# Optimization experiments

Measured on AMD Instinct MI355X. Metric: run time of the kernel, lower is better.

The kernel has to match this reference:

```python
import jax, jax.numpy as jnp
import numpy as np

N = 50000; E = 1600000; H = 128; R = 8; T = 2; P = 1000; M = 223


def setup_inputs() -> dict:
    key = jax.random.key(0)
    ks = jax.random.split(key, 16)
    s = 1.0 / np.sqrt(H).astype(np.float32)
    inp = {}
    inp['neigh_type_count'] = jax.random.uniform(ks[0], (N, 2), dtype=jnp.float32) * 5.0
    inp['norm'] = jax.random.uniform(ks[1], (E,), dtype=jnp.float32) + 0.1
    inp['special_cost'] = jax.random.uniform(ks[2], (N,), dtype=jnp.float32)
    inp['gt_map'] = jax.random.uniform(ks[3], (M, M), dtype=jnp.float32)
    inp['fc_w'] = jax.random.normal(ks[4], (2, H), dtype=jnp.float32) * (1.0 / np.sqrt(2.0))
    inp['fc_b'] = jnp.zeros((H,), jnp.float32)
    inp['w_nt'] = jax.random.normal(ks[5], (T, H, H), dtype=jnp.float32) * s
    inp['w_rel'] = jax.random.normal(ks[6], (R, H, H), dtype=jnp.float32) * s
    inp['fc2_w'] = jax.random.normal(ks[7], (H, 1), dtype=jnp.float32) * s
    inp['fc2_b'] = jnp.zeros((1,), jnp.float32)
    inp['fc3_w'] = jax.random.normal(ks[8], (H, 1), dtype=jnp.float32) * s
    inp['fc3_b'] = jnp.zeros((1,), jnp.float32)
    inp['fl3_w'] = jax.random.normal(ks[9], (H, P), dtype=jnp.float32) * s
    inp['fl3_b'] = jnp.zeros((P,), jnp.float32)
    inp['node_type'] = jax.random.randint(ks[10], (N,), 0, T, dtype=jnp.int32)
    inp['src'] = jax.random.randint(ks[11], (E,), 0, N, dtype=jnp.int32)
    inp['dst'] = jax.random.randint(ks[12], (E,), 0, N, dtype=jnp.int32)
    inp['etype'] = jax.random.randint(ks[13], (E,), 0, R, dtype=jnp.int32)
    return inp


def reference(neigh_type_count, norm, special_cost, gt_map, fc_w, fc_b, w_nt, w_rel,
              fc2_w, fc2_b, fc3_w, fc3_b, fl3_w, fl3_b, node_type, src, dst, etype):
    n = neigh_type_count.shape[0]
    # fc: [N,2] -> [N,H]
    h0 = neigh_type_count @ fc_w + fc_b
    # input RGCN layer: per-src-node-type transform, then per-edge-relation transform.
    # Compute node x type / node x relation products once, then gather per edge
    # (same math as per-edge bmm with gathered weights, far less traffic).
    h_nt_all = jnp.einsum('ni,tio->nto', h0, w_nt)                 # [N,T,H]
    h_nt = jnp.take_along_axis(h_nt_all, node_type[:, None, None].astype(jnp.int32), axis=1)[:, 0, :]  # [N,H]
    h_rel = jnp.einsum('ni,rio->nro', h_nt, w_rel)                 # [N,R,H]
    msg = h_rel[src, etype] * norm[:, None]                        # [E,H]
    h = jax.ops.segment_sum(msg, dst, num_segments=n)              # scatter-sum -> [N,H]
    h = jax.nn.relu(h)                                             # apply_func activation
    # fc2 + clamp(sigmoid)
    pred = jnp.clip(jax.nn.sigmoid(h @ fc2_w + fc2_b), 1e-7, 1e10) # [N,1]
    m = gt_map.shape[0]
    pm = pred[:m * m, 0].reshape(m, m)                             # pred node map [M,M]
    ce = -jnp.sum(gt_map * jnp.log2(pm))                           # min cross-entropy (single GT map)
    rs = jnp.sum(pm, axis=1)                                       # row sums [M]
    cs = jnp.sum(pm, axis=0)                                       # col sums [M]
    loss2 = jnp.sum(pm * (rs[:, None] - pm)) + jnp.sum(pm * (cs[None, :] - pm))
    sumone = jnp.sum((rs - 1.0) ** 2) + jnp.sum((cs - 1.0) ** 2)
    # fc_for_loss3 (sigmoid probs; summed so params get grads)
    prob3_sum = jnp.sum(jax.nn.sigmoid(h @ fl3_w + fl3_b))
    # OutputLayer: scatter-sum src pred_prob to dst, (sum-1)^2 * special_cost
    agg = jax.ops.segment_sum(pred[src, 0], dst, num_segments=n)
    out_cost = jnp.sum(((agg - 1.0) ** 2) * special_cost)
    # dgl.mean_nodes (single graph) + fc3
    gembed = jnp.mean(h, axis=0)
    pred_obj = (gembed @ fc3_w + fc3_b)[0]
    return jnp.stack([pred_obj, sumone, loss2, ce, out_cost, prob3_sum])
```

## Files before the change

### kernel.cpp

```cpp
#include <hip/hip_runtime.h>

#define H 128
#define RNUM 8
#define TNUM 2
#define PNUM 1000
#define MNUM 223
#define BNODES 64
#define NBUCK 782
#define BCAP 2304
#define EPB 4096

typedef __attribute__((ext_vector_type(8))) short bf16x8;
typedef __attribute__((ext_vector_type(4))) float f32x4;

__device__ __forceinline__ float fsig(float z) {
    return 1.0f / (1.0f + __expf(-z));
}
__device__ __forceinline__ float fsig_fast(float z) {
    return __builtin_amdgcn_rcpf(1.0f + __expf(-z));
}

__device__ __forceinline__ float wave_reduce(float v) {
#pragma unroll
    for (int off = 32; off > 0; off >>= 1) v += __shfl_down(v, off, 64);
    return v;
}

__device__ __forceinline__ unsigned short f2bf(float f) {
    unsigned int u = __float_as_uint(f);
    u += 0x7fffu + ((u >> 16) & 1u);
    return (unsigned short)(u >> 16);
}

__global__ __launch_bounds__(512) void partition_setup(
        const int* __restrict__ src, const int* __restrict__ dst,
        const int* __restrict__ etype, const float* __restrict__ norm,
        const int* __restrict__ node_type, int* __restrict__ cursor,
        uint2* __restrict__ buck, int E, int NP,
        const float* __restrict__ fl3_w, const float* __restrict__ fl3_b,
        unsigned short* __restrict__ wt, float* __restrict__ biasws,
        const float* __restrict__ fc_w, const float* __restrict__ fc_b,
        const float* __restrict__ w_nt, const float* __restrict__ w_rel,
        unsigned short* __restrict__ CbT) {
    int blk = blockIdx.x;
    int tid = threadIdx.x;
    if (blk < NP) {
        __shared__ int lh[NBUCK];
        __shared__ int gb[NBUCK];
        for (int i = tid; i < NBUCK; i += 512) lh[i] = 0;
        __syncthreads();
        int base = blk * EPB;
        uint2 pl[8]; int bb[8]; int rk[8];
#pragma unroll
        for (int c = 0; c < 8; ++c) {
            int e = base + c * 512 + tid;
            bb[c] = -1;
            if (e < E) {
                int s = src[e];
                int d = dst[e];
                int r = etype[e];
                float nm = norm[e];
                int t = node_type[s];
                int b = d >> 6;
                int local = d & 63;
                pl[c].x = (unsigned)s | ((unsigned)local << 18) | ((unsigned)r << 24) | ((unsigned)t << 27);
                pl[c].y = __float_as_uint(nm);
                bb[c] = b;
                rk[c] = atomicAdd(&lh[b], 1);
            }
        }
        __syncthreads();
        for (int i = tid; i < NBUCK; i += 512) {
            if (lh[i] > 0) {
                int g = atomicAdd(&cursor[i], lh[i]);
                gb[i] = (g < 0) ? 0 : (g > BCAP ? BCAP : g);
            }
        }
        __syncthreads();
#pragma unroll
        for (int c = 0; c < 8; ++c) {
            if (bb[c] >= 0) {
                int pos = gb[bb[c]] + rk[c];
                if (pos < BCAP) buck[(size_t)bb[c] * BCAP + pos] = pl[c];
            }
        }
    } else if (blk < NP + 256) {
        int p = (blk - NP) * 4 + (tid >> 7);
        int k = tid & 127;
        float v = (p < PNUM) ? fl3_w[(size_t)k * PNUM + p] : 0.0f;
        wt[(size_t)p * H + k] = f2bf(v);
        if (k == 0) biasws[p] = (p < PNUM) ? fl3_b[p] : -1.0e4f;
    } else {
        __shared__ float G[4][3][H];
        int g = tid >> 7;
        int tr = (blk - NP - 256) * 4 + g;
        int t = tr >> 3, r = tr & 7;
        int i = tid & 127;
        float a0 = 0.f, a1 = 0.f, a2 = 0.f;
#pragma unroll 8
        for (int j = 0; j < H; ++j) {
            float w = w_nt[((size_t)t * H + j) * H + i];
            a0 += fc_w[j] * w;
            a1 += fc_w[H + j] * w;
            a2 += fc_b[j] * w;
        }
        G[g][0][i] = a0; G[g][1][i] = a1; G[g][2][i] = a2;
        __syncthreads();
        float c0 = 0.f, c1 = 0.f, c2 = 0.f;
#pragma unroll 8
        for (int k = 0; k < H; ++k) {
            float w = w_rel[((size_t)r * H + k) * H + i];
            c0 += G[g][0][k] * w;
            c1 += G[g][1][k] * w;
            c2 += G[g][2][k] * w;
        }
        CbT[i * 64 + tr * 3 + 0] = f2bf(c0);
        CbT[i * 64 + tr * 3 + 1] = f2bf(c1);
        CbT[i * 64 + tr * 3 + 2] = f2bf(c2);
        if (tr == 0) {
            uint4 z = make_uint4(0u, 0u, 0u, 0u);
            *(uint4*)(CbT + i * 64 + 48) = z;
            *(uint4*)(CbT + i * 64 + 56) = z;
        }
    }
}

__global__ __launch_bounds__(256) void bucket_node(
        const uint2* __restrict__ buck, const int* __restrict__ cursor,
        const float* __restrict__ ntc, const unsigned short* __restrict__ CbT,
        const float* __restrict__ fc2_w, const float* __restrict__ fc2_b,
        unsigned short* __restrict__ hb, float* __restrict__ pred,
        float* __restrict__ gpart, int N) {
    __shared__ float S[64 * 68];
    __shared__ unsigned short Cb[128 * 72];
    __shared__ float gloc[128];
    unsigned long long* P = (unsigned long long*)S;
    int tid = threadIdx.x;
    int bkt = blockIdx.x;
    for (int i = tid; i < 2048; i += 256) S[i] = 0.0f;
    for (int g = tid; g < 1024; g += 256) {
        int row = g >> 3, c = g & 7;
        uint4 v = ((const uint4*)CbT)[g];
        *(uint4*)(Cb + row * 72 + c * 8) = v;
    }
    if (tid < 128) gloc[tid] = 0.0f;
    __syncthreads();

    int cnt = cursor[bkt];
    if (cnt > BCAP) cnt = BCAP;
    if (cnt < 0) cnt = 0;
    const uint2* bp = buck + (size_t)bkt * BCAP;
    for (int base = 0; base < cnt; base += 1024) {
        uint2 pl[4]; float2 cc[4]; int ii[4];
#pragma unroll
        for (int j = 0; j < 4; ++j) {
            ii[j] = base + j * 256 + tid;
            pl[j] = (ii[j] < cnt) ? bp[ii[j]] : make_uint2(0u, 0u);
        }
#pragma unroll
        for (int j = 0; j < 4; ++j)
            cc[j] = (ii[j] < cnt) ? ((const float2*)ntc)[pl[j].x & 0x3FFFF]
                                  : make_float2(0.f, 0.f);
#pragma unroll
        for (int j = 0; j < 4; ++j) {
            if (ii[j] < cnt) {
                int local = (pl[j].x >> 18) & 63;
                int tr = ((pl[j].x >> 24) & 7) + (((pl[j].x >> 27) & 1) << 3);
                float nm = __uint_as_float(pl[j].y);
                unsigned f0 = __float2uint_rn(nm * cc[j].x * 128.0f);
                unsigned f1 = __float2uint_rn(nm * cc[j].y * 128.0f);
                unsigned f2 = __float2uint_rn(nm * 512.0f);
                unsigned long long pk = (unsigned long long)f0
                                      | ((unsigned long long)f1 << 21)
                                      | ((unsigned long long)f2 << 42);
                atomicAdd(&P[local * 16 + tr], pk);
            }
        }
    }
    __syncthreads();

    unsigned long long rpk[4];
#pragma unroll
    for (int u = 0; u < 4; ++u) rpk[u] = P[tid * 4 + u];
    __syncthreads();
#pragma unroll
    for (int u = 0; u < 4; ++u) {
        int idx = tid * 4 + u;
        int local = idx >> 4, tr = idx & 15;
        float* p = S + local * 68 + tr * 3;
        p[0] = (float)(unsigned)(rpk[u] & 0x1FFFFFull) * (1.0f / 128.0f);
        p[1] = (float)(unsigned)((rpk[u] >> 21) & 0x1FFFFFull) * (1.0f / 128.0f);
        p[2] = (float)(unsigned)(rpk[u] >> 42) * (1.0f / 512.0f);
    }
    for (int idx = tid; idx < 1024; idx += 256) {
        int row = idx >> 4, c = idx & 15;
        S[row * 68 + 48 + c] = 0.0f;
    }
    __syncthreads();

    int lane = tid & 63, w = tid >> 6;
    int lrow = lane & 15, quad = lane >> 4;

    bf16x8 a[2];
#pragma unroll
    for (int ks = 0; ks < 2; ++ks) {
        const float* sp = S + (w * 16 + lrow) * 68 + ks * 32 + quad * 8;
        float4 f0 = *(const float4*)sp;
        float4 f1 = *(const float4*)(sp + 4);
        bf16x8 t;
        t[0] = (short)f2bf(f0.x); t[1] = (short)f2bf(f0.y);
        t[2] = (short)f2bf(f0.z); t[3] = (short)f2bf(f0.w);
        t[4] = (short)f2bf(f1.x); t[5] = (short)f2bf(f1.y);
        t[6] = (short)f2bf(f1.z); t[7] = (short)f2bf(f1.w);
        a[ks] = t;
    }

    f32x4 acc[8];
#pragma unroll
    for (int tn = 0; tn < 8; ++tn) acc[tn] = (f32x4){0.f, 0.f, 0.f, 0.f};
#pragma unroll
    for (int ks = 0; ks < 2; ++ks) {
#pragma unroll
        for (int tn = 0; tn < 8; ++tn) {
            bf16x8 b = *(const bf16x8*)(Cb + (tn * 16 + lrow) * 72 + ks * 32 + quad * 8);
            acc[tn] = __builtin_amdgcn_mfma_f32_16x16x32_bf16(a[ks], b, acc[tn], 0, 0, 0);
        }
    }

#pragma unroll
    for (int tn = 0; tn < 8; ++tn)
#pragma unroll
        for (int r = 0; r < 4; ++r) acc[tn][r] = fmaxf(acc[tn][r], 0.f);

    int vbase = bkt * BNODES + w * 16 + quad * 4;
#pragma unroll
    for (int r = 0; r < 4; ++r) {
        unsigned short* hrow = hb + (size_t)(vbase + r) * H + lrow;
#pragma unroll
        for (int tn = 0; tn < 8; ++tn) hrow[tn * 16] = f2bf(acc[tn][r]);
    }
    float pd[4];
#pragma unroll
    for (int r = 0; r < 4; ++r) {
        float s = 0.f;
#pragma unroll
        for (int tn = 0; tn < 8; ++tn) s += acc[tn][r] * fc2_w[tn * 16 + lrow];
        pd[r] = s;
    }
#pragma unroll
    for (int mask = 1; mask < 16; mask <<= 1)
#pragma unroll
        for (int r = 0; r < 4; ++r) pd[r] += __shfl_xor(pd[r], mask, 64);
    if (lrow == 0) {
#pragma unroll
        for (int r = 0; r < 4; ++r) {
            int v = vbase + r;
            if (v < N) {
                float z = pd[r] + fc2_b[0];
                pred[v] = fminf(fmaxf(fsig(z), 1e-7f), 1e10f);
            }
        }
    }
    float csum[8];
#pragma unroll
    for (int tn = 0; tn < 8; ++tn)
        csum[tn] = acc[tn][0] + acc[tn][1] + acc[tn][2] + acc[tn][3];
#pragma unroll
    for (int mask = 16; mask < 64; mask <<= 1)
#pragma unroll
        for (int tn = 0; tn < 8; ++tn) csum[tn] += __shfl_xor(csum[tn], mask, 64);
    if (lane < 16) {
#pragma unroll
        for (int tn = 0; tn < 8; ++tn) atomicAdd(&gloc[tn * 16 + lrow], csum[tn]);
    }
    __syncthreads();
    if (tid < 128) gpart[(size_t)bkt * 128 + tid] = gloc[tid];
}

__global__ __launch_bounds__(256, 2) void mega_kernel(
        const unsigned short* __restrict__ hb, const unsigned short* __restrict__ wt,
        const float* __restrict__ biasws, float* __restrict__ psum, int nb128,
        const uint2* __restrict__ buck, const int* __restrict__ cursor,
        const float* __restrict__ pred, const float* __restrict__ sc,
        const float* __restrict__ gt, float* __restrict__ ocpart, int N,
        float* __restrict__ rs, float* __restrict__ cs,
        float* __restrict__ cepart, float* __restrict__ sqpart,
        const float* __restrict__ gpart, float* __restrict__ gsum, int nbuck) {
    __shared__ unsigned short Bsh[128 * 136];
    __shared__ float red[12];
    int blk = blockIdx.x;
    int tid = threadIdx.x;
    int P1 = 2 * nb128;
    int P2 = P1 + nbuck;
    int P3 = P2 + 2 * MNUM;

    if (blk < P1) {
        int by = blk / nb128, bx = blk - by * nb128;
        int n0 = bx * 128;
        int pt0 = by * 4;
        int lane = tid & 63, wid = tid >> 6;
        int wy = wid >> 1, wx = wid & 1;
        int lrow = lane & 15, quad = lane >> 4;

        bf16x8 a[4][4];
#pragma unroll
        for (int tm = 0; tm < 4; ++tm) {
            const unsigned short* arow = hb + (size_t)(n0 + wy * 64 + tm * 16 + lrow) * H + quad * 8;
#pragma unroll
            for (int ks = 0; ks < 4; ++ks)
                a[tm][ks] = *(const bf16x8*)(arow + ks * 32);
        }

        float lsum = 0.f;
        for (int pi = 0; pi < 4; ++pi) {
            int pt = pt0 + pi;
            __syncthreads();
            {
                int c = tid & 15;
                int r0 = tid >> 4;
#pragma unroll
                for (int it = 0; it < 8; ++it) {
                    int row = r0 + it * 16;
                    uint4 bv = *(const uint4*)(wt + (size_t)(pt * 128 + row) * H + c * 8);
                    *(uint4*)(Bsh + row * 136 + c * 8) = bv;
                }
            }
            __syncthreads();

            f32x4 acc[4][4];
#pragma unroll
            for (int tm = 0; tm < 4; ++tm)
#pragma unroll
                for (int tn = 0; tn < 4; ++tn)
                    acc[tm][tn] = (f32x4){0.f, 0.f, 0.f, 0.f};

            const unsigned short* Bbase = Bsh + (wx * 64 + lrow) * 136 + quad * 8;
#pragma unroll
            for (int ks = 0; ks < 4; ++ks) {
                bf16x8 b[4];
#pragma unroll
                for (int tn = 0; tn < 4; ++tn)
                    b[tn] = *(const bf16x8*)(Bbase + tn * 16 * 136 + ks * 32);
#pragma unroll
                for (int tm = 0; tm < 4; ++tm)
#pragma unroll
                    for (int tn = 0; tn < 4; ++tn)
                        acc[tm][tn] = __builtin_amdgcn_mfma_f32_16x16x32_bf16(a[tm][ks], b[tn], acc[tm][tn], 0, 0, 0);
            }

#pragma unroll
            for (int tn = 0; tn < 4; ++tn) {
                float bv = biasws[pt * 128 + wx * 64 + tn * 16 + lrow];
#pragma unroll
                for (int tm = 0; tm < 4; ++tm) {
#pragma unroll
                    for (int r = 0; r < 4; ++r)
                        lsum += fsig_fast(acc[tm][tn][r] + bv);
                }
            }
        }
        lsum = wave_reduce(lsum);
        if (lane == 0) red[wid] = lsum;
        __syncthreads();
        if (tid == 0)
            psum[by * nb128 + bx] = red[0] + red[1] + red[2] + red[3];
    } else if (blk < P2) {
        int bkt = blk - P1;
        float* agg = (float*)Bsh;
        if (tid < BNODES) agg[tid] = 0.0f;
        __syncthreads();
        int cnt = cursor[bkt];
        if (cnt > BCAP) cnt = BCAP;
        if (cnt < 0) cnt = 0;
        const uint2* bp = buck + (size_t)bkt * BCAP;
        for (int base = 0; base < cnt; base += 2048) {
            unsigned x[8]; float pv[8]; int ii[8];
#pragma unroll
            for (int j = 0; j < 8; ++j) {
                ii[j] = base + j * 256 + tid;
                x[j] = (ii[j] < cnt) ? bp[ii[j]].x : 0u;
            }
#pragma unroll
            for (int j = 0; j < 8; ++j)
                pv[j] = (ii[j] < cnt) ? pred[x[j] & 0x3FFFF] : 0.f;
#pragma unroll
            for (int j = 0; j < 8; ++j)
                if (ii[j] < cnt) atomicAdd(&agg[(x[j] >> 18) & 63], pv[j]);
        }
        __syncthreads();
        if (tid < 64) {
            float v = 0.f;
            int node = bkt * BNODES + tid;
            if (node < N) {
                float d = agg[tid] - 1.0f;
                v = d * d * sc[node];
            }
            v = wave_reduce(v);
            if (tid == 0) ocpart[bkt] = v;
        }
    } else if (blk < P3) {
        int rc = blk - P2;
        if (rc < MNUM) {
            float p = 0.f, ce = 0.f, sq = 0.f;
            if (tid < MNUM) {
                p = pred[rc * MNUM + tid];
                ce = -gt[rc * MNUM + tid] * __log2f(p);
                sq = p * p;
            }
            p = wave_reduce(p);
            ce = wave_reduce(ce);
            sq = wave_reduce(sq);
            int wid = tid >> 6;
            if ((tid & 63) == 0) { red[wid] = p; red[4 + wid] = ce; red[8 + wid] = sq; }
            __syncthreads();
            if (tid == 0) {
                rs[rc] = red[0] + red[1] + red[2] + red[3];
                cepart[rc] = red[4] + red[5] + red[6] + red[7];
                sqpart[rc] = red[8] + red[9] + red[10] + red[11];
            }
        } else {
            int j = rc - MNUM;
            float p = 0.f;
            if (tid < MNUM) p = pred[tid * MNUM + j];
            p = wave_reduce(p);
            if ((tid & 63) == 0) red[tid >> 6] = p;
            __syncthreads();
            if (tid == 0) cs[j] = red[0] + red[1] + red[2] + red[3];
        }
    } else {
        int dim = blk - P3;
        float s = 0.f;
        for (int b = tid; b < nbuck; b += 256) s += gpart[(size_t)b * 128 + dim];
        s = wave_reduce(s);
        if ((tid & 63) == 0) red[tid >> 6] = s;
        __syncthreads();
        if (tid == 0) gsum[dim] = red[0] + red[1] + red[2] + red[3];
    }
}

__global__ void tail_kernel(const float* __restrict__ rs, const float* __restrict__ cs,
                            const float* __restrict__ cepart, const float* __restrict__ sqpart,
                            const float* __restrict__ psum, int npsum,
                            const float* __restrict__ ocpart, int nbuck,
                            const float* __restrict__ gsum, const float* __restrict__ fc3_w,
                            const float* __restrict__ fc3_b, const float* __restrict__ fl3_b,
                            float* __restrict__ out, int N, int padrows) {
    __shared__ float red[4];
    int tid = threadIdx.x;
    float v = 0.f;
    if (tid < MNUM) {
        float a = rs[tid] - 1.0f, b = cs[tid] - 1.0f;
        v = a * a + b * b;
    }
    v = wave_reduce(v);
    if ((tid & 63) == 0) red[tid >> 6] = v;
    __syncthreads();
    if (tid == 0) out[1] = red[0] + red[1] + red[2] + red[3];
    __syncthreads();
    float ce = (tid < MNUM) ? cepart[tid] : 0.f;
    ce = wave_reduce(ce);
    if ((tid & 63) == 0) red[tid >> 6] = ce;
    __syncthreads();
    if (tid == 0) out[3] = red[0] + red[1] + red[2] + red[3];
    __syncthreads();
    float l2 = 0.f;
    if (tid < MNUM)
        l2 = rs[tid] * rs[tid] + cs[tid] * cs[tid] - 2.0f * sqpart[tid];
    l2 = wave_reduce(l2);
    if ((tid & 63) == 0) red[tid >> 6] = l2;
    __syncthreads();
    if (tid == 0) out[2] = red[0] + red[1] + red[2] + red[3];
    __syncthreads();
    float ps = 0.f;
    for (int i = tid; i < npsum; i += 256) ps += psum[i];
    float ss = 0.f;
    for (int p = tid; p < PNUM; p += 256) ss += fsig_fast(fl3_b[p]);
    float comb = ps - (float)padrows * ss;
    comb = wave_reduce(comb);
    if ((tid & 63) == 0) red[tid >> 6] = comb;
    __syncthreads();
    if (tid == 0) out[5] = red[0] + red[1] + red[2] + red[3];
    __syncthreads();
    float oc = 0.f;
    for (int b = tid; b < nbuck; b += 256) oc += ocpart[b];
    oc = wave_reduce(oc);
    if ((tid & 63) == 0) red[tid >> 6] = oc;
    __syncthreads();
    if (tid == 0) out[4] = red[0] + red[1] + red[2] + red[3];
    __syncthreads();
    float pv = 0.f;
    if (tid < 128) pv = gsum[tid] * (1.0f / (float)N) * fc3_w[tid];
    pv = wave_reduce(pv);
    if ((tid & 63) == 0) red[tid >> 6] = pv;
    __syncthreads();
    if (tid == 0) out[0] = red[0] + red[1] + fc3_b[0];
}

extern "C" void kernel_launch(void* const* d_in, const int* in_sizes, int n_in,
                              void* d_out, int out_size, void* d_ws, size_t ws_size,
                              hipStream_t stream) {
    const float* ntc   = (const float*)d_in[0];
    const float* norm  = (const float*)d_in[1];
    const float* sc    = (const float*)d_in[2];
    const float* gt    = (const float*)d_in[3];
    const float* fc_w  = (const float*)d_in[4];
    const float* fc_b  = (const float*)d_in[5];
    const float* w_nt  = (const float*)d_in[6];
    const float* w_rel = (const float*)d_in[7];
    const float* fc2_w = (const float*)d_in[8];
    const float* fc2_b = (const float*)d_in[9];
    const float* fc3_w = (const float*)d_in[10];
    const float* fc3_b = (const float*)d_in[11];
    const float* fl3_w = (const float*)d_in[12];
    const float* fl3_b = (const float*)d_in[13];
    const int* node_type = (const int*)d_in[14];
    const int* src   = (const int*)d_in[15];
    const int* dst   = (const int*)d_in[16];
    const int* etype = (const int*)d_in[17];
    int N = in_sizes[2];
    int E = in_sizes[1];
    int nb128 = (N + 127) / 128;
    int padN  = nb128 * 128;
    int nbuck = padN / BNODES;
    int npsum = nb128 * 2;
    int NP = (E + EPB - 1) / EPB;

    float* ws   = (float*)d_ws;
    unsigned short* wt = (unsigned short*)ws;
    float* biasws = ws + 65536;
    float* gsum = ws + 66560;
    float* rs   = ws + 66688;
    float* cs   = ws + 66944;
    int*  cursor = (int*)(ws + 67200);
    float* psum = ws + 67984;
    float* cepart = ws + 69008;
    float* sqpart = ws + 69264;
    float* ocpart = ws + 69520;
    unsigned short* CbT = (unsigned short*)(ws + 70544);
    float* gpart  = ws + 74640;
    float* pred = ws + 174736;
    unsigned short* hb = (unsigned short*)(pred + N);
    uint2* buck = (uint2*)(hb + (size_t)padN * H);
    float* out  = (float*)d_out;

    hipMemsetAsync(cursor, 0, 784 * sizeof(int), stream);

    partition_setup<<<NP + 260, 512, 0, stream>>>(src, dst, etype, norm, node_type,
                                                  cursor, buck, E, NP,
                                                  fl3_w, fl3_b, wt, biasws,
                                                  fc_w, fc_b, w_nt, w_rel, CbT);
    bucket_node<<<nbuck, 256, 0, stream>>>(buck, cursor, ntc, CbT, fc2_w, fc2_b,
                                           hb, pred, gpart, N);
    int megablocks = 2 * nb128 + nbuck + 2 * MNUM + 128;
    mega_kernel<<<megablocks, 256, 0, stream>>>(hb, wt, biasws, psum, nb128,
                                                buck, cursor, pred, sc, gt, ocpart, N,
                                                rs, cs, cepart, sqpart, gpart, gsum, nbuck);
    tail_kernel<<<1, 256, 0, stream>>>(rs, cs, cepart, sqpart, psum, npsum, ocpart, nbuck,
                                       gsum, fc3_w, fc3_b, fl3_b, out, N, padN - N);
}
```

Measured before the change: 192.9 us.

## Replace dst-bucketing with direct global atomics for edge aggregation

Removes the two-pass bucket partition of edges by destination. Each edge now atomically adds its packed (count, norm) contribution straight into a global per-node, per-type-relation accumulator array, and the output-layer scatter uses global float atomics into a per-node agg array. The fl3 projection loop is merged so one block covers all 8 P-tiles for 128 rows, and the final out_cost reduction moves into a 1024-thread tail kernel. This trades the bucket write and re-read traffic and the cursor atomics for heavy contention from global 64-bit atomics, plus a larger memset of the accumulators.

```diff
diff --git a/kernel.cpp b/kernel.cpp
--- a/kernel.cpp
+++ b/kernel.cpp
@@ -1,13 +1,8 @@
 #include <hip/hip_runtime.h>
 
 #define H 128
-#define RNUM 8
-#define TNUM 2
 #define PNUM 1000
 #define MNUM 223
-#define BNODES 64
-#define NBUCK 782
-#define BCAP 2304
 #define EPB 4096
 
 typedef __attribute__((ext_vector_type(8))) short bf16x8;
@@ -32,11 +27,11 @@
     return (unsigned short)(u >> 16);
 }
 
-__global__ __launch_bounds__(512) void partition_setup(
+__global__ __launch_bounds__(512) void edge_setup(
         const int* __restrict__ src, const int* __restrict__ dst,
         const int* __restrict__ etype, const float* __restrict__ norm,
-        const int* __restrict__ node_type, int* __restrict__ cursor,
-        uint2* __restrict__ buck, int E, int NP,
+        const int* __restrict__ node_type, const float* __restrict__ ntc,
+        unsigned long long* __restrict__ Sg, int E, int NP,
         const float* __restrict__ fl3_w, const float* __restrict__ fl3_b,
         unsigned short* __restrict__ wt, float* __restrict__ biasws,
         const float* __restrict__ fc_w, const float* __restrict__ fc_b,
@@ -45,43 +40,34 @@
     int blk = blockIdx.x;
     int tid = threadIdx.x;
     if (blk < NP) {
-        __shared__ int lh[NBUCK];
-        __shared__ int gb[NBUCK];
-        for (int i = tid; i < NBUCK; i += 512) lh[i] = 0;
-        __syncthreads();
         int base = blk * EPB;
-        uint2 pl[8]; int bb[8]; int rk[8];
+        int s8[8], d8[8], r8[8], ok8[8];
+        float nm8[8];
 #pragma unroll
         for (int c = 0; c < 8; ++c) {
             int e = base + c * 512 + tid;
-            bb[c] = -1;
-            if (e < E) {
-                int s = src[e];
-                int d = dst[e];
-                int r = etype[e];
-                float nm = norm[e];
-                int t = node_type[s];
-                int b = d >> 6;
-                int local = d & 63;
-                pl[c].x = (unsigned)s | ((unsigned)local << 18) | ((unsigned)r << 24) | ((unsigned)t << 27);
-                pl[c].y = __float_as_uint(nm);
-                bb[c] = b;
-                rk[c] = atomicAdd(&lh[b], 1);
-            }
-        }
-        __syncthreads();
-        for (int i = tid; i < NBUCK; i += 512) {
-            if (lh[i] > 0) {
-                int g = atomicAdd(&cursor[i], lh[i]);
-                gb[i] = (g < 0) ? 0 : (g > BCAP ? BCAP : g);
-            }
-        }
-        __syncthreads();
+            ok8[c] = (e < E);
+            s8[c] = ok8[c] ? src[e] : 0;
+            d8[c] = ok8[c] ? dst[e] : 0;
+            r8[c] = ok8[c] ? etype[e] : 0;
+            nm8[c] = ok8[c] ? norm[e] : 0.0f;
+        }
+        int t8[8]; float2 cc8[8];
 #pragma unroll
         for (int c = 0; c < 8; ++c) {
-            if (bb[c] >= 0) {
-                int pos = gb[bb[c]] + rk[c];
-                if (pos < BCAP) buck[(size_t)bb[c] * BCAP + pos] = pl[c];
+            t8[c] = node_type[s8[c]];
+            cc8[c] = ((const float2*)ntc)[s8[c]];
+        }
+#pragma unroll
+        for (int c = 0; c < 8; ++c) {
+            if (ok8[c]) {
+                unsigned f0 = __float2uint_rn(nm8[c] * cc8[c].x * 128.0f);
+                unsigned f1 = __float2uint_rn(nm8[c] * cc8[c].y * 128.0f);
+                unsigned f2 = __float2uint_rn(nm8[c] * 512.0f);
+                unsigned long long pk = (unsigned long long)f0
+                                      | ((unsigned long long)f1 << 21)
+                                      | ((unsigned long long)f2 << 42);
+                atomicAdd(&Sg[(size_t)d8[c] * 16 + r8[c] + (t8[c] << 3)], pk);
             }
         }
     } else if (blk < NP + 256) {
@@ -125,64 +111,28 @@
     }
 }
 
-__global__ __launch_bounds__(256) void bucket_node(
-        const uint2* __restrict__ buck, const int* __restrict__ cursor,
-        const float* __restrict__ ntc, const unsigned short* __restrict__ CbT,
+__global__ __launch_bounds__(256) void node_compute(
+        const unsigned long long* __restrict__ Sg,
+        const unsigned short* __restrict__ CbT,
         const float* __restrict__ fc2_w, const float* __restrict__ fc2_b,
         unsigned short* __restrict__ hb, float* __restrict__ pred,
         float* __restrict__ gpart, int N) {
     __shared__ float S[64 * 68];
     __shared__ unsigned short Cb[128 * 72];
     __shared__ float gloc[128];
-    unsigned long long* P = (unsigned long long*)S;
     int tid = threadIdx.x;
     int bkt = blockIdx.x;
-    for (int i = tid; i < 2048; i += 256) S[i] = 0.0f;
     for (int g = tid; g < 1024; g += 256) {
         int row = g >> 3, c = g & 7;
         uint4 v = ((const uint4*)CbT)[g];
         *(uint4*)(Cb + row * 72 + c * 8) = v;
     }
     if (tid < 128) gloc[tid] = 0.0f;
-    __syncthreads();
-
-    int cnt = cursor[bkt];
-    if (cnt > BCAP) cnt = BCAP;
-    if (cnt < 0) cnt = 0;
-    const uint2* bp = buck + (size_t)bkt * BCAP;
-    for (int base = 0; base < cnt; base += 1024) {
-        uint2 pl[4]; float2 cc[4]; int ii[4];
-#pragma unroll
-        for (int j = 0; j < 4; ++j) {
-            ii[j] = base + j * 256 + tid;
-            pl[j] = (ii[j] < cnt) ? bp[ii[j]] : make_uint2(0u, 0u);
-        }
-#pragma unroll
-        for (int j = 0; j < 4; ++j)
-            cc[j] = (ii[j] < cnt) ? ((const float2*)ntc)[pl[j].x & 0x3FFFF]
-                                  : make_float2(0.f, 0.f);
-#pragma unroll
-        for (int j = 0; j < 4; ++j) {
-            if (ii[j] < cnt) {
-                int local = (pl[j].x >> 18) & 63;
-                int tr = ((pl[j].x >> 24) & 7) + (((pl[j].x >> 27) & 1) << 3);
-                float nm = __uint_as_float(pl[j].y);
-                unsigned f0 = __float2uint_rn(nm * cc[j].x * 128.0f);
-                unsigned f1 = __float2uint_rn(nm * cc[j].y * 128.0f);
-                unsigned f2 = __float2uint_rn(nm * 512.0f);
-                unsigned long long pk = (unsigned long long)f0
-                                      | ((unsigned long long)f1 << 21)
-                                      | ((unsigned long long)f2 << 42);
-                atomicAdd(&P[local * 16 + tr], pk);
-            }
-        }
-    }
-    __syncthreads();
 
     unsigned long long rpk[4];
-#pragma unroll
-    for (int u = 0; u < 4; ++u) rpk[u] = P[tid * 4 + u];
-    __syncthreads();
+    const unsigned long long* sp = Sg + (size_t)bkt * 1024 + tid * 4;
+#pragma unroll
+    for (int u = 0; u < 4; ++u) rpk[u] = sp[u];
 #pragma unroll
     for (int u = 0; u < 4; ++u) {
         int idx = tid * 4 + u;
@@ -204,9 +154,9 @@
     bf16x8 a[2];
 #pragma unroll
     for (int ks = 0; ks < 2; ++ks) {
-        const float* sp = S + (w * 16 + lrow) * 68 + ks * 32 + quad * 8;
-        float4 f0 = *(const float4*)sp;
-        float4 f1 = *(const float4*)(sp + 4);
+        const float* sp2 = S + (w * 16 + lrow) * 68 + ks * 32 + quad * 8;
+        float4 f0 = *(const float4*)sp2;
+        float4 f1 = *(const float4*)(sp2 + 4);
         bf16x8 t;
         t[0] = (short)f2bf(f0.x); t[1] = (short)f2bf(f0.y);
         t[2] = (short)f2bf(f0.z); t[3] = (short)f2bf(f0.w);
@@ -232,7 +182,7 @@
 #pragma unroll
         for (int r = 0; r < 4; ++r) acc[tn][r] = fmaxf(acc[tn][r], 0.f);
 
-    int vbase = bkt * BNODES + w * 16 + quad * 4;
+    int vbase = bkt * 64 + w * 16 + quad * 4;
 #pragma unroll
     for (int r = 0; r < 4; ++r) {
         unsigned short* hrow = hb + (size_t)(vbase + r) * H + lrow;
@@ -280,24 +230,23 @@
 __global__ __launch_bounds__(256, 2) void mega_kernel(
         const unsigned short* __restrict__ hb, const unsigned short* __restrict__ wt,
         const float* __restrict__ biasws, float* __restrict__ psum, int nb128,
-        const uint2* __restrict__ buck, const int* __restrict__ cursor,
-        const float* __restrict__ pred, const float* __restrict__ sc,
-        const float* __restrict__ gt, float* __restrict__ ocpart, int N,
+        const int* __restrict__ src, const int* __restrict__ dst,
+        const float* __restrict__ pred, float* __restrict__ agg, int E,
+        const float* __restrict__ gt, int N,
         float* __restrict__ rs, float* __restrict__ cs,
         float* __restrict__ cepart, float* __restrict__ sqpart,
-        const float* __restrict__ gpart, float* __restrict__ gsum, int nbuck) {
+        const float* __restrict__ gpart, float* __restrict__ gsum,
+        int nbuck, int naggb) {
     __shared__ unsigned short Bsh[128 * 136];
     __shared__ float red[12];
     int blk = blockIdx.x;
     int tid = threadIdx.x;
-    int P1 = 2 * nb128;
-    int P2 = P1 + nbuck;
+    int P1 = nb128;
+    int P2 = P1 + naggb;
     int P3 = P2 + 2 * MNUM;
 
     if (blk < P1) {
-        int by = blk / nb128, bx = blk - by * nb128;
-        int n0 = bx * 128;
-        int pt0 = by * 4;
+        int n0 = blk * 128;
         int lane = tid & 63, wid = tid >> 6;
         int wy = wid >> 1, wx = wid & 1;
         int lrow = lane & 15, quad = lane >> 4;
@@ -312,8 +261,7 @@
         }
 
         float lsum = 0.f;
-        for (int pi = 0; pi < 4; ++pi) {
-            int pt = pt0 + pi;
+        for (int pt = 0; pt < 8; ++pt) {
             __syncthreads();
             {
                 int c = tid & 15;
@@ -363,41 +311,24 @@
         if (lane == 0) red[wid] = lsum;
         __syncthreads();
         if (tid == 0)
-            psum[by * nb128 + bx] = red[0] + red[1] + red[2] + red[3];
+            psum[blk] = red[0] + red[1] + red[2] + red[3];
     } else if (blk < P2) {
-        int bkt = blk - P1;
-        float* agg = (float*)Bsh;
-        if (tid < BNODES) agg[tid] = 0.0f;
-        __syncthreads();
-        int cnt = cursor[bkt];
-        if (cnt > BCAP) cnt = BCAP;
-        if (cnt < 0) cnt = 0;
-        const uint2* bp = buck + (size_t)bkt * BCAP;
-        for (int base = 0; base < cnt; base += 2048) {
-            unsigned x[8]; float pv[8]; int ii[8];
-#pragma unroll
-            for (int j = 0; j < 8; ++j) {
-                ii[j] = base + j * 256 + tid;
-                x[j] = (ii[j] < cnt) ? bp[ii[j]].x : 0u;
-            }
-#pragma unroll
-            for (int j = 0; j < 8; ++j)
-                pv[j] = (ii[j] < cnt) ? pred[x[j] & 0x3FFFF] : 0.f;
-#pragma unroll
-            for (int j = 0; j < 8; ++j)
-                if (ii[j] < cnt) atomicAdd(&agg[(x[j] >> 18) & 63], pv[j]);
-        }
-        __syncthreads();
-        if (tid < 64) {
-            float v = 0.f;
-            int node = bkt * BNODES + tid;
-            if (node < N) {
-                float d = agg[tid] - 1.0f;
-                v = d * d * sc[node];
-            }
-            v = wave_reduce(v);
-            if (tid == 0) ocpart[bkt] = v;
-        }
+        int abk = blk - P1;
+        int base = abk * 2048;
+        int s8[8], d8[8], ok8[8];
+#pragma unroll
+        for (int j = 0; j < 8; ++j) {
+            int e = base + j * 256 + tid;
+            ok8[j] = (e < E);
+            s8[j] = ok8[j] ? src[e] : 0;
+            d8[j] = ok8[j] ? dst[e] : 0;
+        }
+        float pv[8];
+#pragma unroll
+        for (int j = 0; j < 8; ++j) pv[j] = pred[s8[j]];
+#pragma unroll
+        for (int j = 0; j < 8; ++j)
+            if (ok8[j]) atomicAdd(&agg[d8[j]], pv[j]);
     } else if (blk < P3) {
         int rc = blk - P2;
         if (rc < MNUM) {
@@ -438,62 +369,67 @@
     }
 }
 
-__global__ void tail_kernel(const float* __restrict__ rs, const float* __restrict__ cs,
-                            const float* __restrict__ cepart, const float* __restrict__ sqpart,
-                            const float* __restrict__ psum, int npsum,
-                            const float* __restrict__ ocpart, int nbuck,
-                            const float* __restrict__ gsum, const float* __restrict__ fc3_w,
-                            const float* __restrict__ fc3_b, const float* __restrict__ fl3_b,
-                            float* __restrict__ out, int N, int padrows) {
-    __shared__ float red[4];
+__global__ __launch_bounds__(1024) void tail_kernel(
+        const float* __restrict__ rs, const float* __restrict__ cs,
+        const float* __restrict__ cepart, const float* __restrict__ sqpart,
+        const float* __restrict__ psum, int npsum,
+        const float* __restrict__ agg, const float* __restrict__ sc,
+        const float* __restrict__ gsum, const float* __restrict__ fc3_w,
+        const float* __restrict__ fc3_b, const float* __restrict__ fl3_b,
+        float* __restrict__ out, int N, int padrows) {
+    __shared__ float red[16];
     int tid = threadIdx.x;
+    int wid = tid >> 6, lane = tid & 63;
     float v = 0.f;
     if (tid < MNUM) {
         float a = rs[tid] - 1.0f, b = cs[tid] - 1.0f;
         v = a * a + b * b;
     }
     v = wave_reduce(v);
-    if ((tid & 63) == 0) red[tid >> 6] = v;
-    __syncthreads();
-    if (tid == 0) out[1] = red[0] + red[1] + red[2] + red[3];
+    if (lane == 0) red[wid] = v;
+    __syncthreads();
+    if (tid == 0) { float s = 0.f; for (int i = 0; i < 16; ++i) s += red[i]; out[1] = s; }
     __syncthreads();
     float ce = (tid < MNUM) ? cepart[tid] : 0.f;
     ce = wave_reduce(ce);
-    if ((tid & 63) == 0) red[tid >> 6] = ce;
-    __syncthreads();
-    if (tid == 0) out[3] = red[0] + red[1] + red[2] + red[3];
+    if (lane == 0) red[wid] = ce;
+    __syncthreads();
+    if (tid == 0) { float s = 0.f; for (int i = 0; i < 16; ++i) s += red[i]; out[3] = s; }
     __syncthreads();
     float l2 = 0.f;
     if (tid < MNUM)
         l2 = rs[tid] * rs[tid] + cs[tid] * cs[tid] - 2.0f * sqpart[tid];
     l2 = wave_reduce(l2);
-    if ((tid & 63) == 0) red[tid >> 6] = l2;
-    __syncthreads();
-    if (tid == 0) out[2] = red[0] + red[1] + red[2] + red[3];
+    if (lane == 0) red[wid] = l2;
+    __syncthreads();
+    if (tid == 0) { float s = 0.f; for (int i = 0; i < 16; ++i) s += red[i]; out[2] = s; }
     __syncthreads();
     float ps = 0.f;
-    for (int i = tid; i < npsum; i += 256) ps += psum[i];
+    for (int i = tid; i < npsum; i += 1024) ps += psum[i];
     float ss = 0.f;
-    for (int p = tid; p < PNUM; p += 256) ss += fsig_fast(fl3_b[p]);
+    for (int p = tid; p < PNUM; p += 1024) ss += fsig_fast(fl3_b[p]);
     float comb = ps - (float)padrows * ss;
     comb = wave_reduce(comb);
-    if ((tid & 63) == 0) red[tid >> 6] = comb;
-    __syncthreads();
-    if (tid == 0) out[5] = red[0] + red[1] + red[2] + red[3];
+    if (lane == 0) red[wid] = comb;
+    __syncthreads();
+    if (tid == 0) { float s = 0.f; for (int i = 0; i < 16; ++i) s += red[i]; out[5] = s; }
     __syncthreads();
     float oc = 0.f;
-    for (int b = tid; b < nbuck; b += 256) oc += ocpart[b];
+    for (int i = tid; i < N; i += 1024) {
+        float d = agg[i] - 1.0f;
+        oc += d * d * sc[i];
+    }
     oc = wave_reduce(oc);
-    if ((tid & 63) == 0) red[tid >> 6] = oc;
-    __syncthreads();
-    if (tid == 0) out[4] = red[0] + red[1] + red[2] + red[3];
+    if (lane == 0) red[wid] = oc;
+    __syncthreads();
+    if (tid == 0) { float s = 0.f; for (int i = 0; i < 16; ++i) s += red[i]; out[4] = s; }
     __syncthreads();
     float pv = 0.f;
     if (tid < 128) pv = gsum[tid] * (1.0f / (float)N) * fc3_w[tid];
     pv = wave_reduce(pv);
-    if ((tid & 63) == 0) red[tid >> 6] = pv;
-    __syncthreads();
-    if (tid == 0) out[0] = red[0] + red[1] + fc3_b[0];
+    if (lane == 0) red[wid] = pv;
+    __syncthreads();
+    if (tid == 0) { float s = 0.f; for (int i = 0; i < 16; ++i) s += red[i]; out[0] = s + fc3_b[0]; }
 }
 
 extern "C" void kernel_launch(void* const* d_in, const int* in_sizes, int n_in,
@@ -521,9 +457,9 @@
     int E = in_sizes[1];
     int nb128 = (N + 127) / 128;
     int padN  = nb128 * 128;
-    int nbuck = padN / BNODES;
-    int npsum = nb128 * 2;
+    int nbuck = padN / 64;
     int NP = (E + EPB - 1) / EPB;
+    int naggb = (E + 2047) / 2048;
 
     float* ws   = (float*)d_ws;
     unsigned short* wt = (unsigned short*)ws;
@@ -531,30 +467,30 @@
     float* gsum = ws + 66560;
     float* rs   = ws + 66688;
     float* cs   = ws + 66944;
-    int*  cursor = (int*)(ws + 67200);
-    float* psum = ws + 67984;
-    float* cepart = ws + 69008;
-    float* sqpart = ws + 69264;
-    float* ocpart = ws + 69520;
-    unsigned short* CbT = (unsigned short*)(ws + 70544);
-    float* gpart  = ws + 74640;
-    float* pred = ws + 174736;
-    unsigned short* hb = (unsigned short*)(pred + N);
-    uint2* buck = (uint2*)(hb + (size_t)padN * H);
+    float* psum = ws + 67200;
+    float* cepart = ws + 67712;
+    float* sqpart = ws + 67968;
+    unsigned short* CbT = (unsigned short*)(ws + 68224);
+    float* gpart  = ws + 72320;
+    float* pred = ws + 172416;
+    unsigned short* hb = (unsigned short*)(ws + 222416);
+    unsigned long long* Sg = (unsigned long long*)(ws + 3425488);
+    float* agg  = ws + 5027024;
     float* out  = (float*)d_out;
 
-    hipMemsetAsync(cursor, 0, 784 * sizeof(int), stream);
-
-    partition_setup<<<NP + 260, 512, 0, stream>>>(src, dst, etype, norm, node_type,
-                                                  cursor, buck, E, NP,
-                                                  fl3_w, fl3_b, wt, biasws,
-                                                  fc_w, fc_b, w_nt, w_rel, CbT);
-    bucket_node<<<nbuck, 256, 0, stream>>>(buck, cursor, ntc, CbT, fc2_w, fc2_b,
-                                           hb, pred, gpart, N);
-    int megablocks = 2 * nb128 + nbuck + 2 * MNUM + 128;
+    hipMemsetAsync(Sg, 0, (size_t)padN * 16 * 8 + (size_t)padN * 4, stream);
+
+    edge_setup<<<NP + 260, 512, 0, stream>>>(src, dst, etype, norm, node_type, ntc,
+                                             Sg, E, NP,
+                                             fl3_w, fl3_b, wt, biasws,
+                                             fc_w, fc_b, w_nt, w_rel, CbT);
+    node_compute<<<nbuck, 256, 0, stream>>>(Sg, CbT, fc2_w, fc2_b, hb, pred, gpart, N);
+    int megablocks = nb128 + naggb + 2 * MNUM + 128;
     mega_kernel<<<megablocks, 256, 0, stream>>>(hb, wt, biasws, psum, nb128,
-                                                buck, cursor, pred, sc, gt, ocpart, N,
-                                                rs, cs, cepart, sqpart, gpart, gsum, nbuck);
-    tail_kernel<<<1, 256, 0, stream>>>(rs, cs, cepart, sqpart, psum, npsum, ocpart, nbuck,
-                                       gsum, fc3_w, fc3_b, fl3_b, out, N, padN - N);
-}
+                                                src, dst, pred, agg, E,
+                                                gt, N, rs, cs, cepart, sqpart,
+                                                gpart, gsum, nbuck, naggb);
+    tail_kernel<<<1, 1024, 0, stream>>>(rs, cs, cepart, sqpart, psum, nb128,
+                                        agg, sc, gsum, fc3_w, fc3_b, fl3_b,
+                                        out, N, padN - N);
+}
```

Result: slower. 317.7 us (+64.7%).
